# Performance work log

Hardware: AMD Instinct MI355X
Metric: run time of the kernel (lower is better)

## Reference

```python
import jax, jax.numpy as jnp
import numpy as np
from jax import lax

E_NUM, R_NUM = 100000, 500
ENT_DIM = 200
OUT_CH = 16
EPS = 1e-5


def _bn(x, s, b, m, v, axis):
    # eval-mode batchnorm; params broadcast along `axis`
    shape = [1] * x.ndim
    shape[axis] = x.shape[axis]
    s, b, m, v = (p.reshape(shape) for p in (s, b, m, v))
    return (x - m) * (s * lax.rsqrt(v + EPS)) + b


def setup_inputs() -> dict:
    key = jax.random.key(0)
    ks = jax.random.split(key, 12)
    B = 1024
    inp = {
        'entity_id': jax.random.randint(ks[0], (B,), 0, E_NUM),
        'relation_id': jax.random.randint(ks[1], (B,), 0, R_NUM),
        'ent_emb': jax.random.normal(ks[2], (E_NUM, ENT_DIM), jnp.float32) * 0.02,
        'rel_emb': jax.random.normal(ks[3], (R_NUM, ENT_DIM), jnp.float32) * 0.02,
        'filt_w': jax.random.normal(ks[4], (R_NUM, OUT_CH * 9), jnp.float32) * 0.1,
        'filt1_w': jax.random.normal(ks[5], (R_NUM, OUT_CH * 9), jnp.float32) * 0.1,
        'fc_w': jax.random.normal(ks[6], (ENT_DIM, 20 * 20 * OUT_CH * 2), jnp.float32) * 0.01,
        'fc_b': jnp.zeros((ENT_DIM,), jnp.float32),
        'out_bias': jnp.zeros((E_NUM,), jnp.float32),
    }
    for name, c, i in (('bn0', 1, 7), ('bn1', OUT_CH, 8), ('bn2', ENT_DIM, 9)):
        k1, k2, k3 = jax.random.split(ks[i], 3)
        inp[name + '_s'] = 1.0 + 0.1 * jax.random.normal(k1, (c,), jnp.float32)
        inp[name + '_b'] = 0.1 * jax.random.normal(k2, (c,), jnp.float32)
        inp[name + '_m'] = 0.1 * jax.random.normal(k3, (c,), jnp.float32)
        inp[name + '_v'] = jnp.ones((c,), jnp.float32)
    return inp


def reference(entity_id, relation_id, ent_emb, rel_emb, filt_w, filt1_w, fc_w, fc_b,
              out_bias, bn0_s, bn0_b, bn0_m, bn0_v, bn1_s, bn1_b, bn1_m, bn1_v,
              bn2_s, bn2_b, bn2_m, bn2_v):
    B = entity_id.shape[0]
    e = ent_emb[entity_id]                         # [B, 200]
    r = rel_emb[relation_id]                       # [B, 200]
    f = filt_w[relation_id].reshape(B * OUT_CH, 1, 3, 3)
    f1 = filt1_w[relation_id].reshape(B * OUT_CH, 1, 1, 9)

    x = jnp.concatenate([e, r], 1).reshape(B, 1, 10, 40)
    c0, c1, c2, c3 = jnp.split(x, 4, axis=3)       # each [B,1,10,10]
    t1 = jnp.swapaxes(c1, 2, 3)
    t2 = jnp.swapaxes(c3, 2, 3)
    m = jnp.concatenate([c0, c2], 2)               # [B,1,20,10]
    n = jnp.concatenate([t2, t1], 2)               # [B,1,20,10]
    x = jnp.concatenate([m, n], 3)                 # [B,1,20,20]

    x = _bn(x, bn0_s, bn0_b, bn0_m, bn0_v, axis=1)
    x = jnp.transpose(x, (1, 0, 2, 3))             # [1,B,20,20]

    dn = ('NCHW', 'OIHW', 'NCHW')
    x1 = lax.conv_general_dilated(x, f, (1, 1), [(1, 1), (1, 1)],
                                  dimension_numbers=dn, feature_group_count=B)
    x1 = _bn(x1.reshape(B, OUT_CH, 20, 20), bn1_s, bn1_b, bn1_m, bn1_v, axis=1)
    x2 = lax.conv_general_dilated(x, f1, (1, 1), [(0, 0), (4, 4)],
                                  dimension_numbers=dn, feature_group_count=B)
    x2 = _bn(x2.reshape(B, OUT_CH, 20, 20), bn1_s, bn1_b, bn1_m, bn1_v, axis=1)

    x = jax.nn.relu(jnp.concatenate([x1, x2], axis=1)).reshape(B, -1)  # [B,12800]
    x = x @ fc_w.T + fc_b                          # [B,200]
    x = _bn(x, bn2_s, bn2_b, bn2_m, bn2_v, axis=1)
    x = jax.nn.relu(x)
    logits = x @ ent_emb.T + out_bias              # [B, E_NUM]
    return jax.nn.sigmoid(logits)
```

## Files before the change

kernel.cpp:

```cpp
#include <hip/hip_runtime.h>
#include <hip/hip_bf16.h>

#define EPS 1e-5f

typedef __bf16 bf16x8 __attribute__((ext_vector_type(8)));
typedef float f32x4 __attribute__((ext_vector_type(4)));
typedef unsigned short ushort_t;

#define GLDS16(gp, lp) __builtin_amdgcn_global_load_lds( \
    (const __attribute__((address_space(1))) unsigned int*)(gp), \
    (__attribute__((address_space(3))) unsigned int*)(lp), 16, 0, 0)

__device__ __forceinline__ unsigned short f2bf(float f) {
    unsigned int u = __float_as_uint(f);
    u += 0x7fffu + ((u >> 16) & 1u);
    return (unsigned short)(u >> 16);
}

__device__ __forceinline__ void convert_pad_body(
    const float* __restrict__ src, ushort_t* __restrict__ dst,
    int R, int C, int R2, int C2, long long start, long long stride)
{
    int cpr = C2 >> 2;
    long long nchunks = (long long)R2 * cpr;
    for (long long idx = start; idx < nchunks; idx += stride) {
        int row = (int)(idx / cpr);
        int col = ((int)(idx - (long long)row * cpr)) << 2;
        float4 v = make_float4(0.f, 0.f, 0.f, 0.f);
        if (row < R && col < C)
            v = *reinterpret_cast<const float4*>(src + (size_t)row * C + col);
        union { unsigned short h[4]; uint2 u; } pk;
        pk.h[0] = f2bf(v.x); pk.h[1] = f2bf(v.y);
        pk.h[2] = f2bf(v.z); pk.h[3] = f2bf(v.w);
        *reinterpret_cast<uint2*>(dst + (size_t)row * C2 + col) = pk.u;
    }
}

__global__ __launch_bounds__(256) void prep_all_kernel(
    const float* __restrict__ fc_w, ushort_t* __restrict__ fcw,
    const int* __restrict__ eid, const int* __restrict__ rid,
    const float* __restrict__ ent_emb, const float* __restrict__ rel_emb,
    const float* __restrict__ filt_w, const float* __restrict__ filt1_w,
    const float* __restrict__ bn0_s, const float* __restrict__ bn0_b,
    const float* __restrict__ bn0_m, const float* __restrict__ bn0_v,
    const float* __restrict__ bn1_s, const float* __restrict__ bn1_b,
    const float* __restrict__ bn1_m, const float* __restrict__ bn1_v,
    ushort_t* __restrict__ act, ushort_t* __restrict__ E_bf)
{
    __shared__ float img[20][20];
    __shared__ float fA[16][9];
    __shared__ float fB[16][9];
    __shared__ float a1[16], b1[16];

    int t = threadIdx.x;
    if (blockIdx.x >= 4224) {
        long long start = (long long)(blockIdx.x - 4224) * 256 + t;
        convert_pad_body(ent_emb, E_bf, 100000, 200, 100000, 224, start, 21875LL * 256);
        return;
    }
    if (blockIdx.x >= 1024) {
        long long start = (long long)(blockIdx.x - 1024) * 256 + t;
        convert_pad_body(fc_w, fcw, 200, 12800, 256, 12800, start, 3200LL * 256);
        return;
    }

    int b = blockIdx.x;
    int e = eid[b], r = rid[b];

    float a0 = bn0_s[0] * rsqrtf(bn0_v[0] + EPS);
    float c0 = bn0_b[0] - bn0_m[0] * a0;

    for (int p = t; p < 400; p += 256) {
        int i = p / 20, j = p - (p / 20) * 20;
        int src;
        if (i < 10) src = (j < 10) ? (i * 40 + j) : ((j - 10) * 40 + 30 + i);
        else        src = (j < 10) ? ((i - 10) * 40 + 20 + j) : ((j - 10) * 40 + 10 + (i - 10));
        float v = (src < 200) ? ent_emb[(size_t)e * 200 + src]
                              : rel_emb[(size_t)r * 200 + (src - 200)];
        img[i][j] = v * a0 + c0;
    }
    for (int p = t; p < 144; p += 256) fA[p / 9][p % 9] = filt_w[(size_t)r * 144 + p];
    for (int p = t; p < 144; p += 256) fB[p / 9][p % 9] = filt1_w[(size_t)r * 144 + p];
    if (t < 16) {
        float a = bn1_s[t] * rsqrtf(bn1_v[t] + EPS);
        a1[t] = a;
        b1[t] = bn1_b[t] - bn1_m[t] * a;
    }
    __syncthreads();

    for (int idx = t; idx < 12800; idx += 256) {
        int c = idx / 400;
        int p = idx - c * 400;
        int i = p / 20, j = p - (p / 20) * 20;
        int ch = c & 15;
        float acc = 0.f;
        if (c < 16) {
            #pragma unroll
            for (int di = 0; di < 3; ++di) {
                int ii = i + di - 1;
                if (ii < 0 || ii >= 20) continue;
                #pragma unroll
                for (int dj = 0; dj < 3; ++dj) {
                    int jj = j + dj - 1;
                    if (jj >= 0 && jj < 20) acc += img[ii][jj] * fA[ch][di * 3 + dj];
                }
            }
        } else {
            #pragma unroll
            for (int dj = 0; dj < 9; ++dj) {
                int jj = j + dj - 4;
                if (jj >= 0 && jj < 20) acc += img[i][jj] * fB[ch][dj];
            }
        }
        float v = fmaxf(acc * a1[ch] + b1[ch], 0.f);
        act[(size_t)b * 12800 + idx] = f2bf(v);
    }
}

__global__ __launch_bounds__(256) void fc_gemm_kernel(
    const ushort_t* __restrict__ act,
    const ushort_t* __restrict__ fcw,
    float* __restrict__ part)
{
    __shared__ ushort_t lA[128 * 64];
    __shared__ ushort_t lB[64 * 64];

    int t = threadIdx.x;
    int bx = blockIdx.x;
    int mt = bx & 7;
    int nt = (bx >> 3) & 3;
    int ks = bx >> 5;
    int m0 = mt * 128, n0 = nt * 64, k0 = ks * 640;

    int lane = t & 63, w = t >> 6;
    int wm = (w >> 1) * 64;
    int wn = (w & 1) * 32;

    f32x4 acc[4][2] = {};

    for (int step = 0; step < 10; ++step) {
        int kk = k0 + step * 64;
        for (int c = w; c < 16; c += 4) {
            int elem = c * 512 + lane * 8;
            int row = elem >> 6, col = elem & 63;
            GLDS16(act + (size_t)(m0 + row) * 12800 + kk + col, lA + c * 512);
        }
        for (int c = w; c < 8; c += 4) {
            int elem = c * 512 + lane * 8;
            int row = elem >> 6, col = elem & 63;
            GLDS16(fcw + (size_t)(n0 + row) * 12800 + kk + col, lB + c * 512);
        }
        __syncthreads();
        #pragma unroll
        for (int kq = 0; kq < 2; ++kq) {
            bf16x8 af[4], bfr[2];
            #pragma unroll
            for (int mf = 0; mf < 4; ++mf) {
                int row = wm + mf * 16 + (lane & 15);
                af[mf] = *reinterpret_cast<const bf16x8*>(lA + row * 64 + kq * 32 + (lane >> 4) * 8);
            }
            #pragma unroll
            for (int nf = 0; nf < 2; ++nf) {
                int row = wn + nf * 16 + (lane & 15);
                bfr[nf] = *reinterpret_cast<const bf16x8*>(lB + row * 64 + kq * 32 + (lane >> 4) * 8);
            }
            #pragma unroll
            for (int mf = 0; mf < 4; ++mf)
                #pragma unroll
                for (int nf = 0; nf < 2; ++nf)
                    acc[mf][nf] = __builtin_amdgcn_mfma_f32_16x16x32_bf16(af[mf], bfr[nf], acc[mf][nf], 0, 0, 0);
        }
        __syncthreads();
    }

    float* outp = part + (size_t)ks * 1024 * 256;
    #pragma unroll
    for (int mf = 0; mf < 4; ++mf) {
        #pragma unroll
        for (int nf = 0; nf < 2; ++nf) {
            int colg = n0 + wn + nf * 16 + (lane & 15);
            int rowb = (lane >> 4) * 4;
            #pragma unroll
            for (int j = 0; j < 4; ++j) {
                int rowg = m0 + wm + mf * 16 + rowb + j;
                outp[(size_t)rowg * 256 + colg] = acc[mf][nf][j];
            }
        }
    }
}

__global__ __launch_bounds__(256) void reduce_bn2_kernel(
    const float* __restrict__ part, const float* __restrict__ fc_b,
    const float* __restrict__ bn2_s, const float* __restrict__ bn2_b,
    const float* __restrict__ bn2_m, const float* __restrict__ bn2_v,
    ushort_t* __restrict__ h)
{
    int idx = blockIdx.x * 256 + threadIdx.x;
    if (idx >= 1024 * 224) return;
    int m = idx / 224, n = idx - m * 224;
    float v = 0.f;
    if (n < 200) {
        float s = 0.f;
        #pragma unroll 4
        for (int k = 0; k < 20; ++k) s += part[(size_t)k * 1024 * 256 + (size_t)m * 256 + n];
        s += fc_b[n];
        float a = bn2_s[n] * rsqrtf(bn2_v[n] + EPS);
        v = fmaxf((s - bn2_m[n]) * a + bn2_b[n], 0.f);
    }
    h[idx] = f2bf(v);
}

__global__ __launch_bounds__(256) void big_gemm_kernel(
    const ushort_t* __restrict__ hm,
    const ushort_t* __restrict__ em,
    const float* __restrict__ out_bias,
    float* __restrict__ out)
{
    __shared__ ushort_t lA[2][64 * 32];
    __shared__ ushort_t lB[2][128 * 32];
    __shared__ float tr[32][68];

    int phys = blockIdx.x;
    int virt = (phys & 7) * 1564 + (phys >> 3);
    int mt = virt & 15;
    int nt = virt >> 4;
    int m0 = mt * 64, n0 = nt * 128;

    int t = threadIdx.x;
    int lane = t & 63, w = t >> 6;
    int wm = (w >> 1) * 32;
    int wn = (w & 1) * 64;
    int srow = (lane >> 2);
    int scol = ((lane & 3) ^ ((srow >> 1) & 3)) * 8;

    f32x4 acc[2][4] = {};

    if (w < 4) {
        int row = w * 16 + srow;
        GLDS16(hm + (size_t)(m0 + row) * 224 + scol, lA[0] + w * 512);
    }
    for (int c = w; c < 8; c += 4) {
        int row = c * 16 + srow;
        int rowB = n0 + row; if (rowB > 99999) rowB = 99999;
        GLDS16(em + (size_t)rowB * 224 + scol, lB[0] + c * 512);
    }
    __syncthreads();

    for (int step = 0; step < 7; ++step) {
        int cur = step & 1;
        if (step < 6) {
            int kk = (step + 1) * 32;
            int nxt = cur ^ 1;
            if (w < 4) {
                int row = w * 16 + srow;
                GLDS16(hm + (size_t)(m0 + row) * 224 + kk + scol, lA[nxt] + w * 512);
            }
            for (int c = w; c < 8; c += 4) {
                int row = c * 16 + srow;
                int rowB = n0 + row; if (rowB > 99999) rowB = 99999;
                GLDS16(em + (size_t)rowB * 224 + kk + scol, lB[nxt] + c * 512);
            }
        }
        const ushort_t* A = lA[cur];
        const ushort_t* B = lB[cur];
        bf16x8 af[2], bfr[4];
        #pragma unroll
        for (int mf = 0; mf < 2; ++mf) {
            int r = wm + mf * 16 + (lane & 15);
            int pc = ((lane >> 4) ^ ((r >> 1) & 3)) * 8;
            af[mf] = *reinterpret_cast<const bf16x8*>(A + r * 32 + pc);
        }
        #pragma unroll
        for (int nf = 0; nf < 4; ++nf) {
            int r = wn + nf * 16 + (lane & 15);
            int pc = ((lane >> 4) ^ ((r >> 1) & 3)) * 8;
            bfr[nf] = *reinterpret_cast<const bf16x8*>(B + r * 32 + pc);
        }
        #pragma unroll
        for (int mf = 0; mf < 2; ++mf)
            #pragma unroll
            for (int nf = 0; nf < 4; ++nf)
                acc[mf][nf] = __builtin_amdgcn_mfma_f32_16x16x32_bf16(bfr[nf], af[mf], acc[mf][nf], 0, 0, 0);
        __syncthreads();
    }

    int ncol_base = n0 + wn + (lane >> 4) * 4;
    f32x4 b4[4];
    #pragma unroll
    for (int nf = 0; nf < 4; ++nf) {
        int colg = ncol_base + nf * 16;
        b4[nf] = (colg < 100000) ? *reinterpret_cast<const f32x4*>(out_bias + colg)
                                 : f32x4{0.f, 0.f, 0.f, 0.f};
    }
    int lr = (w >> 1) * 16 + (lane & 15);
    int lc4 = (lane >> 4) * 4;
    bool first = true;
    #pragma unroll
    for (int h = 0; h < 2; ++h) {
        #pragma unroll
        for (int c = 0; c < 2; ++c) {
            if (!first) __syncthreads();
            first = false;
            if ((w & 1) == c) {
                #pragma unroll
                for (int nf = 0; nf < 4; ++nf) {
                    f32x4 x = acc[h][nf];
                    f32x4 s;
                    #pragma unroll
                    for (int q = 0; q < 4; ++q)
                        s[q] = __builtin_amdgcn_rcpf(1.f + __expf(-(x[q] + b4[nf][q])));
                    *reinterpret_cast<f32x4*>(&tr[lr][lc4 + nf * 16]) = s;
                }
            }
            __syncthreads();
            #pragma unroll
            for (int p = 0; p < 2; ++p) {
                int sl = (t >> 4) + p * 16;
                int grow = m0 + (sl >> 4) * 32 + h * 16 + (sl & 15);
                int gcol = n0 + c * 64 + (t & 15) * 4;
                f32x4 v = *reinterpret_cast<const f32x4*>(&tr[sl][(t & 15) * 4]);
                if (gcol < 100000)
                    __builtin_nontemporal_store(v, reinterpret_cast<f32x4*>(out + (size_t)grow * 100000 + gcol));
            }
        }
    }
}

extern "C" void kernel_launch(void* const* d_in, const int* in_sizes, int n_in,
                              void* d_out, int out_size, void* d_ws, size_t ws_size,
                              hipStream_t stream)
{
    const int*   eid      = (const int*)d_in[0];
    const int*   rid      = (const int*)d_in[1];
    const float* ent_emb  = (const float*)d_in[2];
    const float* rel_emb  = (const float*)d_in[3];
    const float* filt_w   = (const float*)d_in[4];
    const float* filt1_w  = (const float*)d_in[5];
    const float* fc_w     = (const float*)d_in[6];
    const float* fc_b     = (const float*)d_in[7];
    const float* out_bias = (const float*)d_in[8];
    const float* bn0_s = (const float*)d_in[9];
    const float* bn0_b = (const float*)d_in[10];
    const float* bn0_m = (const float*)d_in[11];
    const float* bn0_v = (const float*)d_in[12];
    const float* bn1_s = (const float*)d_in[13];
    const float* bn1_b = (const float*)d_in[14];
    const float* bn1_m = (const float*)d_in[15];
    const float* bn1_v = (const float*)d_in[16];
    const float* bn2_s = (const float*)d_in[17];
    const float* bn2_b = (const float*)d_in[18];
    const float* bn2_m = (const float*)d_in[19];
    const float* bn2_v = (const float*)d_in[20];
    float* out = (float*)d_out;

    char* ws = (char*)d_ws;
    ushort_t* E_bf = (ushort_t*)(ws + 0);
    ushort_t* act  = (ushort_t*)(ws + 44800000);
    ushort_t* fcw  = (ushort_t*)(ws + 71014400);
    float*    part = (float*)(ws + 77568000);
    ushort_t* hmat = (ushort_t*)(ws + 98539520);

    hipLaunchKernelGGL(prep_all_kernel, dim3(1024 + 3200 + 21875), dim3(256), 0, stream,
                       fc_w, fcw,
                       eid, rid, ent_emb, rel_emb, filt_w, filt1_w,
                       bn0_s, bn0_b, bn0_m, bn0_v, bn1_s, bn1_b, bn1_m, bn1_v, act, E_bf);
    hipLaunchKernelGGL(fc_gemm_kernel, dim3(640), dim3(256), 0, stream,
                       act, fcw, part);
    hipLaunchKernelGGL(reduce_bn2_kernel, dim3((1024 * 224) / 256), dim3(256), 0, stream,
                       part, fc_b, bn2_s, bn2_b, bn2_m, bn2_v, hmat);
    hipLaunchKernelGGL(big_gemm_kernel, dim3(12512), dim3(256), 0, stream,
                       hmat, E_bf, out_bias, out);
}
```

Measured before the change: 185.0 us.

## Fuse entity-embedding bf16 conversion into big GEMM B-tile staging

```diff
diff --git a/kernel.cpp b/kernel.cpp
--- a/kernel.cpp
+++ b/kernel.cpp
@@ -6,6 +6,8 @@
 typedef __bf16 bf16x8 __attribute__((ext_vector_type(8)));
 typedef float f32x4 __attribute__((ext_vector_type(4)));
 typedef unsigned short ushort_t;
+typedef unsigned int uint32_t_;
+typedef uint32_t_ u32x4 __attribute__((ext_vector_type(4)));
 
 #define GLDS16(gp, lp) __builtin_amdgcn_global_load_lds( \
     (const __attribute__((address_space(1))) unsigned int*)(gp), \
@@ -15,6 +17,10 @@
     unsigned int u = __float_as_uint(f);
     u += 0x7fffu + ((u >> 16) & 1u);
     return (unsigned short)(u >> 16);
+}
+
+__device__ __forceinline__ unsigned int pack2bf(float a, float b) {
+    return (unsigned int)f2bf(a) | ((unsigned int)f2bf(b) << 16);
 }
 
 __device__ __forceinline__ void convert_pad_body(
@@ -45,7 +51,7 @@
     const float* __restrict__ bn0_m, const float* __restrict__ bn0_v,
     const float* __restrict__ bn1_s, const float* __restrict__ bn1_b,
     const float* __restrict__ bn1_m, const float* __restrict__ bn1_v,
-    ushort_t* __restrict__ act, ushort_t* __restrict__ E_bf)
+    ushort_t* __restrict__ act)
 {
     __shared__ float img[20][20];
     __shared__ float fA[16][9];
@@ -53,11 +59,6 @@
     __shared__ float a1[16], b1[16];
 
     int t = threadIdx.x;
-    if (blockIdx.x >= 4224) {
-        long long start = (long long)(blockIdx.x - 4224) * 256 + t;
-        convert_pad_body(ent_emb, E_bf, 100000, 200, 100000, 224, start, 21875LL * 256);
-        return;
-    }
     if (blockIdx.x >= 1024) {
         long long start = (long long)(blockIdx.x - 1024) * 256 + t;
         convert_pad_body(fc_w, fcw, 200, 12800, 256, 12800, start, 3200LL * 256);
@@ -212,7 +213,7 @@
 
 __global__ __launch_bounds__(256) void big_gemm_kernel(
     const ushort_t* __restrict__ hm,
-    const ushort_t* __restrict__ em,
+    const float* __restrict__ emf,
     const float* __restrict__ out_bias,
     float* __restrict__ out)
 {
@@ -235,15 +236,31 @@
 
     f32x4 acc[2][4] = {};
 
+    #define STAGE_B(kk_, buf_) { \
+        _Pragma("unroll") \
+        for (int c = w; c < 8; c += 4) { \
+            int r_ = c * 16 + srow; \
+            int rowB_ = n0 + r_; if (rowB_ > 99999) rowB_ = 99999; \
+            int gc_ = ((lane & 3) ^ ((r_ >> 1) & 3)) * 8 + (kk_); \
+            f32x4 v0_ = {0.f,0.f,0.f,0.f}, v1_ = {0.f,0.f,0.f,0.f}; \
+            if (gc_ < 200) { \
+                const float* p_ = emf + (size_t)rowB_ * 200 + gc_; \
+                v0_ = *reinterpret_cast<const f32x4*>(p_); \
+                v1_ = *reinterpret_cast<const f32x4*>(p_ + 4); \
+            } \
+            u32x4 pk_; \
+            pk_[0] = pack2bf(v0_[0], v0_[1]); \
+            pk_[1] = pack2bf(v0_[2], v0_[3]); \
+            pk_[2] = pack2bf(v1_[0], v1_[1]); \
+            pk_[3] = pack2bf(v1_[2], v1_[3]); \
+            *reinterpret_cast<u32x4*>(lB[buf_] + c * 512 + lane * 8) = pk_; \
+        } }
+
     if (w < 4) {
         int row = w * 16 + srow;
         GLDS16(hm + (size_t)(m0 + row) * 224 + scol, lA[0] + w * 512);
     }
-    for (int c = w; c < 8; c += 4) {
-        int row = c * 16 + srow;
-        int rowB = n0 + row; if (rowB > 99999) rowB = 99999;
-        GLDS16(em + (size_t)rowB * 224 + scol, lB[0] + c * 512);
-    }
+    STAGE_B(0, 0);
     __syncthreads();
 
     for (int step = 0; step < 7; ++step) {
@@ -255,11 +272,7 @@
                 int row = w * 16 + srow;
                 GLDS16(hm + (size_t)(m0 + row) * 224 + kk + scol, lA[nxt] + w * 512);
             }
-            for (int c = w; c < 8; c += 4) {
-                int row = c * 16 + srow;
-                int rowB = n0 + row; if (rowB > 99999) rowB = 99999;
-                GLDS16(em + (size_t)rowB * 224 + kk + scol, lB[nxt] + c * 512);
-            }
+            STAGE_B(kk, nxt);
         }
         const ushort_t* A = lA[cur];
         const ushort_t* B = lB[cur];
@@ -324,6 +337,7 @@
             }
         }
     }
+    #undef STAGE_B
 }
 
 extern "C" void kernel_launch(void* const* d_in, const int* in_sizes, int n_in,
@@ -354,20 +368,19 @@
     float* out = (float*)d_out;
 
     char* ws = (char*)d_ws;
-    ushort_t* E_bf = (ushort_t*)(ws + 0);
     ushort_t* act  = (ushort_t*)(ws + 44800000);
     ushort_t* fcw  = (ushort_t*)(ws + 71014400);
     float*    part = (float*)(ws + 77568000);
     ushort_t* hmat = (ushort_t*)(ws + 98539520);
 
-    hipLaunchKernelGGL(prep_all_kernel, dim3(1024 + 3200 + 21875), dim3(256), 0, stream,
+    hipLaunchKernelGGL(prep_all_kernel, dim3(1024 + 3200), dim3(256), 0, stream,
                        fc_w, fcw,
                        eid, rid, ent_emb, rel_emb, filt_w, filt1_w,
-                       bn0_s, bn0_b, bn0_m, bn0_v, bn1_s, bn1_b, bn1_m, bn1_v, act, E_bf);
+                       bn0_s, bn0_b, bn0_m, bn0_v, bn1_s, bn1_b, bn1_m, bn1_v, act);
     hipLaunchKernelGGL(fc_gemm_kernel, dim3(640), dim3(256), 0, stream,
                        act, fcw, part);
     hipLaunchKernelGGL(reduce_bn2_kernel, dim3((1024 * 224) / 256), dim3(256), 0, stream,
                        part, fc_b, bn2_s, bn2_b, bn2_m, bn2_v, hmat);
     hipLaunchKernelGGL(big_gemm_kernel, dim3(12512), dim3(256), 0, stream,
-                       hmat, E_bf, out_bias, out);
-}
+                       hmat, ent_emb, out_bias, out);
+}
```

Result: slower. 218.0 us (+17.8%).
